# Optimization experiments

Measured on AMD Instinct MI355X. Metric: run time of the kernel, lower is better.

Reference implementation:

```python
import jax, jax.numpy as jnp
import numpy as np
from jax import lax

B, T, DE, DT = 64, 511, 400, 100
D = DE + DT              # encoder + tag embedding concat
S = T + 1                # head sentinel prepended
HG, HE, M = 384, 64, 32  # graph hidden, edge hidden, band width


def lstm_layer(x, h0, c0, Wih, Whh, bih, bhh):
    """x: [N, L, in] -> [N, L, H]; torch LSTM gate order (i, f, g, o)."""
    def step(carry, xt):
        h, c = carry
        gates = xt @ Wih.T + bih + h @ Whh.T + bhh
        i, f, g, o = jnp.split(gates, 4, axis=-1)
        c = jax.nn.sigmoid(f) * c + jax.nn.sigmoid(i) * jnp.tanh(g)
        h = jax.nn.sigmoid(o) * jnp.tanh(c)
        return (h, c), h
    _, ys = lax.scan(step, (h0, c0), jnp.swapaxes(x, 0, 1))
    return jnp.swapaxes(ys, 0, 1)


def setup_inputs() -> dict:
    key = jax.random.key(0)
    ks = jax.random.split(key, 32)
    def u(k, shape, h):
        s = 1.0 / np.sqrt(h)
        return jax.random.uniform(k, shape, jnp.float32, -s, s)
    return {
        "input": jax.random.normal(ks[0], (B, T, DE), jnp.float32),
        "tag_embeddings": jax.random.normal(ks[1], (B, T, DT), jnp.float32),
        "mask": jnp.ones((B, T), jnp.int32),
        "head_indices": jax.random.randint(ks[2], (B, T), 0, S),
        "head_sentinel": jax.random.normal(ks[3], (D,), jnp.float32),
        "bos_past": jnp.zeros((1,), jnp.float32),
        # graph LSTM (2 layers, dropout inactive at eval)
        "g_Wih0": u(ks[4], (4 * HG, D), HG),  "g_Whh0": u(ks[5], (4 * HG, HG), HG),
        "g_bih0": u(ks[6], (4 * HG,), HG),     "g_bhh0": u(ks[7], (4 * HG,), HG),
        "g_Wih1": u(ks[8], (4 * HG, HG), HG),  "g_Whh1": u(ks[9], (4 * HG, HG), HG),
        "g_bih1": u(ks[10], (4 * HG,), HG),    "g_bhh1": u(ks[11], (4 * HG,), HG),
        # edge LSTM past (2 layers, input size 1)
        "e_Wih0": u(ks[12], (4 * HE, 1), HE),  "e_Whh0": u(ks[13], (4 * HE, HE), HE),
        "e_bih0": u(ks[14], (4 * HE,), HE),    "e_bhh0": u(ks[15], (4 * HE,), HE),
        "e_Wih1": u(ks[16], (4 * HE, HE), HE), "e_Whh1": u(ks[17], (4 * HE, HE), HE),
        "e_bih1": u(ks[18], (4 * HE,), HE),    "e_bhh1": u(ks[19], (4 * HE,), HE),
        "g2e_W": u(ks[20], (HE, HG), HG),      "g2e_b": u(ks[21], (HE,), HG),
        "cls_W": u(ks[22], (1, HE), HE),       "cls_b": u(ks[23], (1,), HE),
        "ht_W": u(ks[24], (DT, HG), HG),       "ht_b": u(ks[25], (DT,), HG),
        "dt_W": u(ks[26], (DT, HG), HG),       "dt_b": u(ks[27], (DT,), HG),
    }


def reference(input, tag_embeddings, mask, head_indices, head_sentinel, bos_past,
              g_Wih0, g_Whh0, g_bih0, g_bhh0, g_Wih1, g_Whh1, g_bih1, g_bhh1,
              e_Wih0, e_Whh0, e_bih0, e_bhh0, e_Wih1, e_Whh1, e_bih1, e_bhh1,
              g2e_W, g2e_b, cls_W, cls_b, ht_W, ht_b, dt_W, dt_b):
    # --- sentinel prepend + adjust_for_sentinel ---
    x = jnp.concatenate([input, tag_embeddings], axis=-1)                      # [B,T,D]
    x = jnp.concatenate([jnp.broadcast_to(head_sentinel, (B, 1, D)), x], 1)    # [B,S,D]
    mask_s = jnp.concatenate([jnp.ones((B, 1), mask.dtype), mask], axis=1)
    heads = jnp.concatenate([jnp.zeros((B, 1), head_indices.dtype), head_indices], axis=1)
    # --- packed graph LSTM (2 layers, zero init); pad_packed zeros masked positions ---
    zg = jnp.zeros((B, HG), x.dtype)
    h = lstm_layer(x, zg, zg, g_Wih0, g_Whh0, g_bih0, g_bhh0)
    graph_state = lstm_layer(h, zg, zg, g_Wih1, g_Whh1, g_bih1, g_bhh1)        # [B,S,HG]
    graph_state = graph_state * mask_s[..., None].astype(graph_state.dtype)
    # --- edge_pass_train (split=False): teacher-forced banded edge LSTM ---
    proj = graph_state.reshape(B * S, HG) @ g2e_W.T + g2e_b                    # [B*S,HE]
    Lm = min(M, S)
    A_sq = jax.nn.one_hot(heads, S, dtype=jnp.float32)                         # adj_indices_to_adj_matrix
    A_in = A_sq[:, :, :Lm].reshape(B * S, Lm, 1)                               # make_adj_sequence band
    bos = jnp.broadcast_to(bos_past.reshape(1, 1, 1), (B * S, 1, 1))
    A_in = jnp.concatenate([bos, A_in], axis=1)                                # [B*S,Lm+1,1]
    ze = jnp.zeros((B * S, HE), proj.dtype)
    e = lstm_layer(A_in, proj, ze, e_Wih0, e_Whh0, e_bih0, e_bhh0)             # h0=proj per layer, c0=0
    e = lstm_layer(e, proj, ze, e_Wih1, e_Whh1, e_bih1, e_bhh1)
    edge_logits = e @ cls_W.T + cls_b                                          # [B*S,Lm+1,1]
    Ap = edge_logits[:, 1:, 0].reshape(B, S, Lm)                               # drop bos step
    # banded writeback: arc_logits[:, i, :min(S,M)] = Ap[:, i, :] for every i
    arc_logits = jnp.zeros((B, S, S), graph_state.dtype).at[:, :, :Lm].set(Ap)
    # --- tag feedforwards (dropout = identity at eval) ---
    head_tag = jax.nn.elu(graph_state @ ht_W.T + ht_b)
    dep_tag = jax.nn.elu(graph_state @ dt_W.T + dt_b)
    return arc_logits, head_tag, dep_tag
```

## Files before the change

kernel.cpp:

```cpp
#include <hip/hip_runtime.h>
#include <hip/hip_bf16.h>
#include <stdint.h>

#define BB   64
#define TT   511
#define SS   512
#define DD   500
#define KXP  512
#define HG   384
#define G4   1536
#define HE   64
#define E4   256
#define NSEQ (BB*SS)

typedef __hip_bfloat16 bf16;
typedef float  floatx4 __attribute__((ext_vector_type(4)));
typedef int    intx4   __attribute__((ext_vector_type(4)));
typedef __bf16 bfrag8  __attribute__((ext_vector_type(8)));

static __device__ __forceinline__ floatx4 MFMA16(bfrag8 a, bfrag8 b, floatx4 c){
  return __builtin_amdgcn_mfma_f32_16x16x32_bf16(a, b, c, 0, 0, 0);
}
static __device__ __forceinline__ float sigm_(float x){ return 1.f/(1.f + __expf(-x)); }
static __device__ __forceinline__ float tanh_(float x){
  x = fminf(fmaxf(x, -15.f), 15.f);
  float e = __expf(2.f*x);
  return (e - 1.f)/(e + 1.f);
}
static __device__ __forceinline__ float actv(float x, bool isg){
  float s = 1.f/(1.f + __expf(isg ? -2.f*x : -x));
  return isg ? (2.f*s - 1.f) : s;
}
static __device__ __forceinline__ float b2f(unsigned short u){
  union { unsigned int i; float f; } x; x.i = ((unsigned int)u)<<16; return x.f;
}
static __device__ __forceinline__ unsigned short f2bu(float f){
  bf16 b = __float2bfloat16(f);
  return *reinterpret_cast<unsigned short*>(&b);
}
static __device__ __forceinline__ bfrag8 asfrag(intx4 v){
  union { intx4 i; bfrag8 f; } u; u.i = v; return u.f;
}

static __device__ __forceinline__ bfrag8 ldfrag_coh(const bf16* p){
  unsigned long long u0 = __hip_atomic_load((const unsigned long long*)p,     __ATOMIC_RELAXED, __HIP_MEMORY_SCOPE_SYSTEM);
  unsigned long long u1 = __hip_atomic_load((const unsigned long long*)p + 1, __ATOMIC_RELAXED, __HIP_MEMORY_SCOPE_SYSTEM);
  union { unsigned long long u[2]; bfrag8 f; } x; x.u[0]=u0; x.u[1]=u1;
  return x.f;
}
static __device__ __forceinline__ void stpair_coh(bf16* p, float lo, float hi){
  unsigned int pk = (unsigned int)f2bu(lo) | ((unsigned int)f2bu(hi) << 16);
  __hip_atomic_store((unsigned int*)p, pk, __ATOMIC_RELAXED, __HIP_MEMORY_SCOPE_SYSTEM);
}

__global__ __launch_bounds__(256) void prep_x(const float* __restrict__ input,
    const float* __restrict__ tag, const float* __restrict__ sent,
    bf16* __restrict__ Xb)
{
  const size_t stp = (size_t)gridDim.x * blockDim.x;
  for (size_t i = (size_t)blockIdx.x*blockDim.x + threadIdx.x; i < (size_t)NSEQ*KXP; i += stp){
    int m = (int)(i >> 9), k = (int)(i & 511);
    int b = m >> 9, s = m & 511;
    float v;
    if (k >= DD)        v = 0.f;
    else if (s == 0)    v = sent[k];
    else if (k < 400)   v = input[(size_t)(b*TT + s-1)*400 + k];
    else                v = tag  [(size_t)(b*TT + s-1)*100 + (k-400)];
    Xb[i] = __float2bfloat16(v);
  }
}

__global__ __launch_bounds__(256) void prep_w(
  const float* __restrict__ gWih0, const float* __restrict__ gWhh0,
  const float* __restrict__ gbih0, const float* __restrict__ gbhh0,
  const float* __restrict__ gWih1, const float* __restrict__ gWhh1,
  const float* __restrict__ gbih1, const float* __restrict__ gbhh1,
  const float* __restrict__ eWih0, const float* __restrict__ eWhh0,
  const float* __restrict__ ebih0, const float* __restrict__ ebhh0,
  const float* __restrict__ eWih1, const float* __restrict__ eWhh1,
  const float* __restrict__ ebih1, const float* __restrict__ ebhh1,
  const float* __restrict__ g2eW, const float* __restrict__ htW, const float* __restrict__ dtW,
  bf16* __restrict__ W0i, bf16* __restrict__ W0r, bf16* __restrict__ W1c,
  float* __restrict__ gb0, float* __restrict__ gb1,
  bf16* __restrict__ eW0b, bf16* __restrict__ eW1ab, bf16* __restrict__ eW1bb,
  float* __restrict__ eb0, float* __restrict__ eb1, float* __restrict__ ew0cv,
  bf16* __restrict__ g2eWb, bf16* __restrict__ htWb, bf16* __restrict__ dtWb)
{
  const int st = blockIdx.x*blockDim.x + threadIdx.x;
  const int gs = gridDim.x*blockDim.x;
  for (int i=st; i<G4*KXP; i+=gs){ int n=i>>9, k=i&511; int j=n>>2, g=n&3;
      W0i[i] = __float2bfloat16(k<DD ? gWih0[(size_t)(g*HG+j)*DD+k] : 0.f); }
  for (int i=st; i<G4*HG; i+=gs){ int n=i/HG, k=i-n*HG; int j=n>>2, g=n&3;
      W0r[i] = __float2bfloat16(gWhh0[(size_t)(g*HG+j)*HG+k]); }
  for (int i=st; i<G4*768; i+=gs){ int n=i/768, k=i-n*768; int j=n>>2, g=n&3;
      W1c[i] = __float2bfloat16(k<HG ? gWih1[(size_t)(g*HG+j)*HG+k]
                                     : gWhh1[(size_t)(g*HG+j)*HG+(k-HG)]); }
  for (int i=st; i<G4; i+=gs){ int j=i>>2, g=i&3; int s=g*HG+j;
      gb0[i]=gbih0[s]+gbhh0[s]; gb1[i]=gbih1[s]+gbhh1[s]; }
  for (int i=st; i<E4*HE; i+=gs){ eW0b[i]=__float2bfloat16(eWhh0[i]);
      eW1ab[i]=__float2bfloat16(eWih1[i]); eW1bb[i]=__float2bfloat16(eWhh1[i]); }
  for (int i=st; i<E4; i+=gs){ eb0[i]=ebih0[i]+ebhh0[i]; eb1[i]=ebih1[i]+ebhh1[i];
      ew0cv[i]=eWih0[i]; }
  for (int i=st; i<HE*HG; i+=gs) g2eWb[i]=__float2bfloat16(g2eW[i]);
  for (int i=st; i<128*HG; i+=gs){
      htWb[i] = __float2bfloat16(i<100*HG ? htW[i] : 0.f);
      dtWb[i] = __float2bfloat16(i<100*HG ? dtW[i] : 0.f); }
}

template<int KTOT,int BN,int WAVES_M,int WAVES_N,int EPI>
__global__ __launch_bounds__(256) void gemm_mfma(
    const bf16* __restrict__ A, const bf16* __restrict__ Wt,
    const float* __restrict__ bias, const int* __restrict__ mask,
    void* __restrict__ outp, int Nreal)
{
  constexpr int WMT = 128/(WAVES_M*16);
  constexpr int WNT = BN /(WAVES_N*16);
  __shared__ alignas(16) bf16 As[128][32];
  __shared__ alignas(16) bf16 Bs[BN][32];
  const int tid = threadIdx.x;
  const int bm = blockIdx.x & 255, bn = blockIdx.x >> 8;
  const int m0 = bm*128, n0 = bn*BN;
  const int wid = tid>>6, l = tid&63, lj = l&15, lq = l>>4;
  const int wm = wid / WAVES_N, wn = wid % WAVES_N;
  floatx4 acc[WMT][WNT] = {};
  for (int k0 = 0; k0 < KTOT; k0 += 32){
    __syncthreads();
    for (int c = tid; c < 128*4; c += 256){
      int row = c>>2, ch = c&3;
      *(uint4*)&As[row][ch*8] = *(const uint4*)&A[(size_t)(m0+row)*KTOT + k0 + ch*8];
    }
    for (int c = tid; c < BN*4; c += 256){
      int row = c>>2, ch = c&3;
      *(uint4*)&Bs[row][ch*8] = *(const uint4*)&Wt[(size_t)(n0+row)*KTOT + k0 + ch*8];
    }
    __syncthreads();
    bfrag8 af[WMT]; bfrag8 bfr[WNT];
    #pragma unroll
    for (int mi=0;mi<WMT;++mi) af[mi]  = *(const bfrag8*)&As[wm*WMT*16 + mi*16 + lj][lq*8];
    #pragma unroll
    for (int ni=0;ni<WNT;++ni) bfr[ni] = *(const bfrag8*)&Bs[wn*WNT*16 + ni*16 + lj][lq*8];
    #pragma unroll
    for (int mi=0;mi<WMT;++mi)
      #pragma unroll
      for (int ni=0;ni<WNT;++ni)
        acc[mi][ni] = MFMA16(af[mi], bfr[ni], acc[mi][ni]);
  }
  #pragma unroll
  for (int mi=0;mi<WMT;++mi){
    #pragma unroll
    for (int ni=0;ni<WNT;++ni){
      #pragma unroll
      for (int r=0;r<4;++r){
        int grow = m0 + wm*WMT*16 + mi*16 + 4*lq + r;
        int gcol = n0 + wn*WNT*16 + ni*16 + lj;
        float v = acc[mi][ni][r];
        if (EPI == 0){
          v += bias[gcol];
          ((bf16*)outp)[(size_t)grow*Nreal + gcol] = __float2bfloat16(v);
        } else if (EPI == 3){
          v += bias[gcol];
          int s = grow & 511, b = grow >> 9;
          ((bf16*)outp)[((size_t)s*BB + b)*G4 + gcol] = __float2bfloat16(v);
        } else {
          int s = grow & 511, b = grow >> 9;
          float mk = (s==0) ? 1.f : (float)mask[b*TT + s - 1];
          v = v*mk + bias[gcol];
          if (EPI == 1){
            ((bf16*)outp)[(size_t)grow*Nreal + gcol] = __float2bfloat16(v);
          } else {
            v = v > 0.f ? v : expm1f(v);
            if (gcol < Nreal) ((float*)outp)[(size_t)grow*Nreal + gcol] = v;
          }
        }
      }
    }
  }
}

template<int IS1>
__device__ __forceinline__ void rnn_body(int bid, int tid,
    const bf16* __restrict__ G0t, const bf16* __restrict__ Wsrc,
    const float* __restrict__ gb1,
    bf16* __restrict__ h0seq, bf16* __restrict__ h1seq, unsigned int* __restrict__ flags)
{
  constexpr int KW = IS1 ? 768 : 384;
  constexpr int KF = IS1 ? 24 : 12;
  const int bl = IS1 ? bid-48 : bid;
  const int w = tid>>6, l = tid&63, lj = l&15, lq = l>>4;
  const int m0 = w*16;
  const int n0 = bl*32;
  const int a  = lj>>2;
  const int gl = l&3;
  const bool isg = (gl==2);

  intx4 Wr0[KF], Wr1[KF];
  #pragma unroll
  for (int kf=0; kf<KF; ++kf){
    Wr0[kf] = *(const intx4*)&Wsrc[(size_t)(n0 + lj)*KW      + kf*32 + lq*8];
    Wr1[kf] = *(const intx4*)&Wsrc[(size_t)(n0 + 16 + lj)*KW + kf*32 + lq*8];
  }
  #pragma unroll
  for (int kf=0; kf<KF; ++kf)
    asm volatile("" : "+v"(Wr0[kf]), "+v"(Wr1[kf]));

  float bi0 = 0.f, bi1 = 0.f;
  if (IS1){ bi0 = gb1[n0 + 4*a + gl]; bi1 = gb1[n0 + 16 + 4*a + gl]; }

  float c0s[4]={0,0,0,0}, c1s[4]={0,0,0,0};
  unsigned short g0pre[2][4];
  if (!IS1){
    #pragma unroll
    for (int nt=0;nt<2;++nt)
      #pragma unroll
      for (int r=0;r<4;++r)
        g0pre[nt][r] = *(const unsigned short*)&G0t[(size_t)(m0 + 4*lq + r)*G4 + n0 + nt*16 + 4*a + gl];
  }
  unsigned int* myflag = flags + (size_t)(((IS1?48:0) + bl)*4 + w)*16;
  unsigned int* f0p = flags + (size_t)((l)*4 + w)*16;
  unsigned int* f1p = flags + (size_t)((48 + l)*4 + w)*16;

  const int ITMAX = IS1 ? SS : (SS-1);
  for (int it=0; it<=ITMAX; ++it){
    if (it >= 1){
      const unsigned tgt = (unsigned)it;
      const bool need = (l < 48);
      while (true){
        bool ok = true;
        if (need){
          unsigned f0 = __hip_atomic_load(f0p, __ATOMIC_RELAXED, __HIP_MEMORY_SCOPE_AGENT);
          ok = (f0 >= tgt);
          if (IS1){
            unsigned f1 = __hip_atomic_load(f1p, __ATOMIC_RELAXED, __HIP_MEMORY_SCOPE_AGENT);
            ok = ok && (f1 >= tgt);
          }
        }
        if (__all(ok)) break;
        __builtin_amdgcn_s_sleep(1);
      }
      asm volatile("" ::: "memory");
    }
    if (!IS1 || it >= 1){
      const int t = IS1 ? it-1 : it;
      bfrag8 ha[KF];
      if (IS1){
        const bf16* hb0 = h0seq + ((size_t)t*BB + (m0+lj))*HG;
        #pragma unroll
        for (int kf=0;kf<12;++kf) ha[kf] = ldfrag_coh(hb0 + kf*32 + lq*8);
        if (t > 0){
          const bf16* hb1 = h1seq + ((size_t)(m0+lj)*SS + (t-1))*HG;
          #pragma unroll
          for (int kf=12;kf<24;++kf) ha[kf] = ldfrag_coh(hb1 + (kf-12)*32 + lq*8);
        }
      } else if (t > 0){
        const bf16* hb = h0seq + ((size_t)(t-1)*BB + (m0+lj))*HG;
        #pragma unroll
        for (int kf=0;kf<12;++kf) ha[kf] = ldfrag_coh(hb + kf*32 + lq*8);
      }
      floatx4 aA0={0,0,0,0}, aB0={0,0,0,0}, aA1={0,0,0,0}, aB1={0,0,0,0};
      if (IS1 || t > 0){
        #pragma unroll
        for (int kf=0;kf<12;++kf){
          if (kf&1){ aB0 = MFMA16(ha[kf], asfrag(Wr0[kf]), aB0); aB1 = MFMA16(ha[kf], asfrag(Wr1[kf]), aB1); }
          else     { aA0 = MFMA16(ha[kf], asfrag(Wr0[kf]), aA0); aA1 = MFMA16(ha[kf], asfrag(Wr1[kf]), aA1); }
        }
      }
      if (IS1 && t > 0){
        #pragma unroll
        for (int kf=12;kf<24;++kf){
          if (kf&1){ aB0 = MFMA16(ha[kf], asfrag(Wr0[kf]), aB0); aB1 = MFMA16(ha[kf], asfrag(Wr1[kf]), aB1); }
          else     { aA0 = MFMA16(ha[kf], asfrag(Wr0[kf]), aA0); aA1 = MFMA16(ha[kf], asfrag(Wr1[kf]), aA1); }
        }
      }
      const floatx4 s0 = aA0 + aB0, s1 = aA1 + aB1;
      #pragma unroll
      for (int nt=0; nt<2; ++nt){
        #pragma unroll
        for (int r=0; r<4; ++r){
          float x = nt ? s1[r] : s0[r];
          x += IS1 ? (nt ? bi1 : bi0) : b2f(g0pre[nt][r]);
          float av = actv(x, isg);
          float i_ = __shfl(av, (l&60)|0);
          float f_ = __shfl(av, (l&60)|1);
          float g_ = __shfl(av, (l&60)|2);
          float o_ = __shfl(av, (l&60)|3);
          float cp = nt ? c1s[r] : c0s[r];
          float c = f_*cp + i_*g_;
          if (nt) c1s[r] = c; else c0s[r] = c;
          float h = o_*tanh_(c);
          float hn = __shfl(h, l^4);
          if ((l&7) == 0){
            int bb = m0 + 4*lq + r;
            int jh = bl*8 + nt*4 + a;
            bf16* hp = IS1 ? (h1seq + ((size_t)bb*SS + t)*HG + jh)
                           : (h0seq + ((size_t)t*BB + bb)*HG + jh);
            stpair_coh(hp, h, hn);
          }
        }
      }
    }
    asm volatile("s_waitcnt vmcnt(0)" ::: "memory");
    if (l == 0)
      __hip_atomic_store(myflag, (unsigned)(it+1),
                         __ATOMIC_RELAXED, __HIP_MEMORY_SCOPE_AGENT);
    if (!IS1 && it+1 <= ITMAX){
      #pragma unroll
      for (int nt=0;nt<2;++nt)
        #pragma unroll
        for (int r=0;r<4;++r)
          g0pre[nt][r] = *(const unsigned short*)&G0t[((size_t)(it+1)*BB + m0 + 4*lq + r)*G4 + n0 + nt*16 + 4*a + gl];
    }
  }
}

__global__ __launch_bounds__(256,1) void graph_rnn(
    const bf16* __restrict__ G0t, const bf16* __restrict__ W0r, const bf16* __restrict__ W1c,
    const float* __restrict__ gb1, bf16* __restrict__ h0seq, bf16* __restrict__ h1seq,
    unsigned int* flags)
{
  if (blockIdx.x < 48) rnn_body<0>(blockIdx.x, threadIdx.x, G0t, W0r, gb1, h0seq, h1seq, flags);
  else                 rnn_body<1>(blockIdx.x, threadIdx.x, G0t, W1c, gb1, h0seq, h1seq, flags);
}

__global__ __launch_bounds__(256) void edge_lstm(
    const bf16* __restrict__ projb,
    const bf16* __restrict__ eW0b, const bf16* __restrict__ eW1ab, const bf16* __restrict__ eW1bb,
    const float* __restrict__ eb0, const float* __restrict__ eb1, const float* __restrict__ ew0c,
    const float* __restrict__ clsW, const float* __restrict__ clsb_p, const float* __restrict__ bos_p,
    const int* __restrict__ heads, float* __restrict__ arc)
{
  __shared__ alignas(16) bf16 hbuf0[16][72];
  __shared__ alignas(16) bf16 hbuf1[16][72];
  __shared__ float lbuf[4][16];
  const int tid = threadIdx.x, w = tid>>6, l = tid&63, lj = l&15, lq = l>>4;
  const int seq0 = blockIdx.x * 16;
  const int jglob = w*16 + lj;
  for (int i = tid; i < 16*64; i += 256){
    int sl = i >> 6, jj = i & 63;
    bf16 v = projb[(size_t)(seq0+sl)*HE + jj];
    hbuf0[sl][jj] = v; hbuf1[sl][jj] = v;
  }
  bfrag8 W0f[4][2], W1af[4][2], W1bf[4][2];
  #pragma unroll
  for (int g=0; g<4; ++g){
    #pragma unroll
    for (int kk=0; kk<2; ++kk){
      size_t offw = (size_t)(g*HE + jglob)*HE + kk*32 + lq*8;
      W0f [g][kk] = *(const bfrag8*)&eW0b [offw];
      W1af[g][kk] = *(const bfrag8*)&eW1ab[offw];
      W1bf[g][kk] = *(const bfrag8*)&eW1bb[offw];
    }
  }
  float ebr0[4], ebr1[4], ewr[4];
  #pragma unroll
  for (int g=0; g<4; ++g){ ebr0[g]=eb0[g*HE+jglob]; ebr1[g]=eb1[g*HE+jglob]; ewr[g]=ew0c[g*HE+jglob]; }
  const float clswj = clsW[jglob];
  const float bos = bos_p[0], clsb = clsb_p[0];
  int hd[4]; float c0r[4]={0,0,0,0}, c1r[4]={0,0,0,0};
  #pragma unroll
  for (int r=0;r<4;++r){
    int sq = seq0 + 4*lq + r;
    int b = sq >> 9, s = sq & 511;
    hd[r] = (s==0) ? 0 : heads[b*TT + s - 1];
  }
  __syncthreads();
  for (int j=0; j<33; ++j){
    floatx4 acc0[4] = {};
    bfrag8 a0[2];
    #pragma unroll
    for (int kk=0; kk<2; ++kk)
      a0[kk] = *(const bfrag8*)((const char*)&hbuf0[0][0] + lj*144 + kk*64 + lq*16);
    #pragma unroll
    for (int g=0; g<4; ++g)
      #pragma unroll
      for (int kk=0; kk<2; ++kk)
        acc0[g] = MFMA16(a0[kk], W0f[g][kk], acc0[g]);
    __syncthreads();
    float h0v[4];
    #pragma unroll
    for (int r=0;r<4;++r){
      float x = (j==0) ? bos : ((hd[r] == j-1) ? 1.f : 0.f);
      float pi = acc0[0][r] + ebr0[0] + x*ewr[0];
      float pf = acc0[1][r] + ebr0[1] + x*ewr[1];
      float pg = acc0[2][r] + ebr0[2] + x*ewr[2];
      float po = acc0[3][r] + ebr0[3] + x*ewr[3];
      float i_=sigm_(pi), f_=sigm_(pf), g_=tanh_(pg), o_=sigm_(po);
      c0r[r] = f_*c0r[r] + i_*g_;
      h0v[r] = o_*tanh_(c0r[r]);
    }
    #pragma unroll
    for (int r=0;r<4;++r) hbuf0[4*lq + r][jglob] = __float2bfloat16(h0v[r]);
    __syncthreads();
    floatx4 acc1[4] = {};
    bfrag8 a1[2], a2[2];
    #pragma unroll
    for (int kk=0;kk<2;++kk){
      a1[kk] = *(const bfrag8*)((const char*)&hbuf0[0][0] + lj*144 + kk*64 + lq*16);
      a2[kk] = *(const bfrag8*)((const char*)&hbuf1[0][0] + lj*144 + kk*64 + lq*16);
    }
    #pragma unroll
    for (int g=0; g<4; ++g){
      #pragma unroll
      for (int kk=0;kk<2;++kk){
        acc1[g] = MFMA16(a1[kk], W1af[g][kk], acc1[g]);
        acc1[g] = MFMA16(a2[kk], W1bf[g][kk], acc1[g]);
      }
    }
    __syncthreads();
    float p[4];
    #pragma unroll
    for (int r=0;r<4;++r){
      float pi = acc1[0][r] + ebr1[0];
      float pf = acc1[1][r] + ebr1[1];
      float pg = acc1[2][r] + ebr1[2];
      float po = acc1[3][r] + ebr1[3];
      float i_=sigm_(pi), f_=sigm_(pf), g_=tanh_(pg), o_=sigm_(po);
      c1r[r] = f_*c1r[r] + i_*g_;
      float h1 = o_*tanh_(c1r[r]);
      hbuf1[4*lq + r][jglob] = __float2bfloat16(h1);
      p[r] = h1 * clswj;
    }
    #pragma unroll
    for (int mk=1; mk<16; mk<<=1)
      #pragma unroll
      for (int r=0;r<4;++r) p[r] += __shfl_xor(p[r], mk, 64);
    if (lj == 0){
      #pragma unroll
      for (int r=0;r<4;++r) lbuf[w][4*lq + r] = p[r];
    }
    __syncthreads();
    if (tid < 16 && j >= 1){
      int sq = seq0 + tid;
      float v = lbuf[0][tid] + lbuf[1][tid] + lbuf[2][tid] + lbuf[3][tid] + clsb;
      arc[(size_t)sq*SS + (j-1)] = v;
    }
  }
}

extern "C" void kernel_launch(void* const* d_in, const int* in_sizes, int n_in,
                              void* d_out, int out_size, void* d_ws, size_t ws_size,
                              hipStream_t stream)
{
  const float* input = (const float*)d_in[0];
  const float* tag   = (const float*)d_in[1];
  const int*   mask  = (const int*)  d_in[2];
  const int*   heads = (const int*)  d_in[3];
  const float* sent  = (const float*)d_in[4];
  const float* bosp  = (const float*)d_in[5];
  const float* gWih0 = (const float*)d_in[6];
  const float* gWhh0 = (const float*)d_in[7];
  const float* gbih0 = (const float*)d_in[8];
  const float* gbhh0 = (const float*)d_in[9];
  const float* gWih1 = (const float*)d_in[10];
  const float* gWhh1 = (const float*)d_in[11];
  const float* gbih1 = (const float*)d_in[12];
  const float* gbhh1 = (const float*)d_in[13];
  const float* eWih0 = (const float*)d_in[14];
  const float* eWhh0 = (const float*)d_in[15];
  const float* ebih0 = (const float*)d_in[16];
  const float* ebhh0 = (const float*)d_in[17];
  const float* eWih1 = (const float*)d_in[18];
  const float* eWhh1 = (const float*)d_in[19];
  const float* ebih1 = (const float*)d_in[20];
  const float* ebhh1 = (const float*)d_in[21];
  const float* g2eW  = (const float*)d_in[22];
  const float* g2eb  = (const float*)d_in[23];
  const float* clsW  = (const float*)d_in[24];
  const float* clsb  = (const float*)d_in[25];
  const float* htW   = (const float*)d_in[26];
  const float* htb   = (const float*)d_in[27];
  const float* dtW   = (const float*)d_in[28];
  const float* dtb   = (const float*)d_in[29];

  char* wsb = (char*)d_ws;
  size_t off = 0;
  auto take = [&](size_t bytes)->char* {
    char* p = wsb + off;
    off = (off + bytes + 255) & ~(size_t)255;
    return p;
  };
  bf16*  Xb     = (bf16*) take((size_t)NSEQ*KXP*2);
  bf16*  W0i    = (bf16*) take((size_t)G4*KXP*2);
  bf16*  W0r    = (bf16*) take((size_t)G4*HG*2);
  bf16*  W1c    = (bf16*) take((size_t)G4*768*2);
  float* gb0i   = (float*)take(G4*4);
  float* gb1i   = (float*)take(G4*4);
  bf16*  G0t    = (bf16*) take((size_t)NSEQ*G4*2);
  bf16*  h0seq  = (bf16*) take((size_t)SS*BB*HG*2);
  bf16*  h1seq  = (bf16*) take((size_t)NSEQ*HG*2);
  unsigned int* flags = (unsigned int*)take(384*16*4);
  bf16*  projb  = (bf16*) take((size_t)NSEQ*HE*2);
  bf16*  eW0b   = (bf16*) take(E4*HE*2);
  bf16*  eW1ab  = (bf16*) take(E4*HE*2);
  bf16*  eW1bb  = (bf16*) take(E4*HE*2);
  float* eb0w   = (float*)take(E4*4);
  float* eb1w   = (float*)take(E4*4);
  float* ew0cw  = (float*)take(E4*4);
  bf16*  g2eWb  = (bf16*) take(HE*HG*2);
  bf16*  htWb   = (bf16*) take(128*HG*2);
  bf16*  dtWb   = (bf16*) take(128*HG*2);

  (void)hipMemsetAsync(d_out, 0, (size_t)16777216*4, stream);
  (void)hipMemsetAsync(flags, 0, 384*16*4, stream);

  prep_x<<<2048,256,0,stream>>>(input, tag, sent, Xb);
  prep_w<<<512,256,0,stream>>>(gWih0,gWhh0,gbih0,gbhh0,gWih1,gWhh1,gbih1,gbhh1,
                               eWih0,eWhh0,ebih0,ebhh0,eWih1,eWhh1,ebih1,ebhh1,
                               g2eW,htW,dtW,
                               W0i,W0r,W1c,gb0i,gb1i,eW0b,eW1ab,eW1bb,
                               eb0w,eb1w,ew0cw,g2eWb,htWb,dtWb);

  gemm_mfma<KXP,128,2,2,3><<<3072,256,0,stream>>>(Xb, W0i, gb0i, nullptr, (void*)G0t, G4);

  graph_rnn<<<96,256,0,stream>>>(G0t, W0r, W1c, gb1i, h0seq, h1seq, flags);

  gemm_mfma<HG,64,4,1,1><<<256,256,0,stream>>>(h1seq, g2eWb, g2eb, mask, (void*)projb, HE);

  edge_lstm<<<2048,256,0,stream>>>(projb, eW0b, eW1ab, eW1bb, eb0w, eb1w, ew0cw,
                                   clsW, clsb, bosp, heads, (float*)d_out);

  gemm_mfma<HG,128,2,2,2><<<256,256,0,stream>>>(h1seq, htWb, htb, mask,
      (void*)((float*)d_out + 16777216), 100);
  gemm_mfma<HG,128,2,2,2><<<256,256,0,stream>>>(h1seq, dtWb, dtb, mask,
      (void*)((float*)d_out + 16777216 + 3276800), 100);
}
```

Before: 4.936 ms.

## Overlap layer-0 input GEMM with recurrent LSTM via flags; fuse post GEMMs

Moves the layer-0 input-projection GEMM into the persistent graph_rnn launch as extra worker blocks that process timestep pairs in order. Each worker publishes a per-tile flag, and the recurrent blocks wait on those flags before reading G0t, so the projection overlaps the sequential recurrence instead of running before it. It also merges the three post-RNN GEMMs into a single launch and vectorises the prep_x and prep_w conversion loops. The risk is that correctness now depends on the RNN blocks being resident and progressing while they spin on flags, and there is extra flag polling and memory traffic from the system-scope stores.

After: 5.184 ms. 1.05x slower.

```diff
diff --git a/kernel.cpp b/kernel.cpp
--- a/kernel.cpp
+++ b/kernel.cpp
@@ -17,6 +17,7 @@
 typedef float  floatx4 __attribute__((ext_vector_type(4)));
 typedef int    intx4   __attribute__((ext_vector_type(4)));
 typedef __bf16 bfrag8  __attribute__((ext_vector_type(8)));
+typedef unsigned short ushort8 __attribute__((ext_vector_type(8)));
 
 static __device__ __forceinline__ floatx4 MFMA16(bfrag8 a, bfrag8 b, floatx4 c){
   return __builtin_amdgcn_mfma_f32_16x16x32_bf16(a, b, c, 0, 0, 0);
@@ -52,21 +53,49 @@
   unsigned int pk = (unsigned int)f2bu(lo) | ((unsigned int)f2bu(hi) << 16);
   __hip_atomic_store((unsigned int*)p, pk, __ATOMIC_RELAXED, __HIP_MEMORY_SCOPE_SYSTEM);
 }
+static __device__ __forceinline__ unsigned int ld32_sys(const bf16* p){
+  return __hip_atomic_load((const unsigned int*)p, __ATOMIC_RELAXED, __HIP_MEMORY_SCOPE_SYSTEM);
+}
+static __device__ __forceinline__ void st32_sys(bf16* p, unsigned int v){
+  __hip_atomic_store((unsigned int*)p, v, __ATOMIC_RELAXED, __HIP_MEMORY_SCOPE_SYSTEM);
+}
 
 __global__ __launch_bounds__(256) void prep_x(const float* __restrict__ input,
     const float* __restrict__ tag, const float* __restrict__ sent,
     bf16* __restrict__ Xb)
 {
+  const size_t N8 = (size_t)NSEQ*KXP/8;
   const size_t stp = (size_t)gridDim.x * blockDim.x;
-  for (size_t i = (size_t)blockIdx.x*blockDim.x + threadIdx.x; i < (size_t)NSEQ*KXP; i += stp){
-    int m = (int)(i >> 9), k = (int)(i & 511);
+  for (size_t i8 = (size_t)blockIdx.x*blockDim.x + threadIdx.x; i8 < N8; i8 += stp){
+    int m = (int)(i8 >> 6);
+    int k = ((int)i8 & 63) * 8;
     int b = m >> 9, s = m & 511;
-    float v;
-    if (k >= DD)        v = 0.f;
-    else if (s == 0)    v = sent[k];
-    else if (k < 400)   v = input[(size_t)(b*TT + s-1)*400 + k];
-    else                v = tag  [(size_t)(b*TT + s-1)*100 + (k-400)];
-    Xb[i] = __float2bfloat16(v);
+    float v[8];
+    if (s == 0){
+      #pragma unroll
+      for (int j=0;j<8;++j) v[j] = (k+j < DD) ? sent[k+j] : 0.f;
+    } else if (k < 400){
+      const float* src = input + (size_t)(b*TT + s-1)*400 + k;
+      float4 a = *(const float4*)src;
+      float4 c = *(const float4*)(src+4);
+      v[0]=a.x; v[1]=a.y; v[2]=a.z; v[3]=a.w; v[4]=c.x; v[5]=c.y; v[6]=c.z; v[7]=c.w;
+    } else if (k < 496){
+      const float* src = tag + (size_t)(b*TT + s-1)*100 + (k-400);
+      float4 a = *(const float4*)src;
+      float4 c = *(const float4*)(src+4);
+      v[0]=a.x; v[1]=a.y; v[2]=a.z; v[3]=a.w; v[4]=c.x; v[5]=c.y; v[6]=c.z; v[7]=c.w;
+    } else if (k == 496){
+      const float* src = tag + (size_t)(b*TT + s-1)*100 + 96;
+      float4 a = *(const float4*)src;
+      v[0]=a.x; v[1]=a.y; v[2]=a.z; v[3]=a.w; v[4]=0.f; v[5]=0.f; v[6]=0.f; v[7]=0.f;
+    } else {
+      #pragma unroll
+      for (int j=0;j<8;++j) v[j]=0.f;
+    }
+    ushort8 o;
+    #pragma unroll
+    for (int j=0;j<8;++j) o[j] = f2bu(v[j]);
+    *(ushort8*)&Xb[i8*8] = o;
   }
 }
 
@@ -88,27 +117,40 @@
 {
   const int st = blockIdx.x*blockDim.x + threadIdx.x;
   const int gs = gridDim.x*blockDim.x;
-  for (int i=st; i<G4*KXP; i+=gs){ int n=i>>9, k=i&511; int j=n>>2, g=n&3;
-      W0i[i] = __float2bfloat16(k<DD ? gWih0[(size_t)(g*HG+j)*DD+k] : 0.f); }
-  for (int i=st; i<G4*HG; i+=gs){ int n=i/HG, k=i-n*HG; int j=n>>2, g=n&3;
-      W0r[i] = __float2bfloat16(gWhh0[(size_t)(g*HG+j)*HG+k]); }
-  for (int i=st; i<G4*768; i+=gs){ int n=i/768, k=i-n*768; int j=n>>2, g=n&3;
-      W1c[i] = __float2bfloat16(k<HG ? gWih1[(size_t)(g*HG+j)*HG+k]
-                                     : gWhh1[(size_t)(g*HG+j)*HG+(k-HG)]); }
+  auto cvt4 = [](const float* s)->ushort4 {
+    float4 f = *(const float4*)s;
+    ushort4 u; u.x=f2bu(f.x); u.y=f2bu(f.y); u.z=f2bu(f.z); u.w=f2bu(f.w); return u;
+  };
+  for (int i4=st; i4<G4*KXP/4; i4+=gs){ int n=i4>>7, kk=(i4&127)*4; int j=n>>2, g=n&3;
+      ushort4 u;
+      if (kk < DD) u = cvt4(&gWih0[(size_t)(g*HG+j)*DD + kk]);
+      else { u.x=u.y=u.z=u.w=0; }
+      *(ushort4*)&W0i[(size_t)i4*4] = u; }
+  for (int i4=st; i4<G4*HG/4; i4+=gs){ int n=i4/96, kk=(i4%96)*4; int j=n>>2, g=n&3;
+      *(ushort4*)&W0r[(size_t)i4*4] = cvt4(&gWhh0[(size_t)(g*HG+j)*HG + kk]); }
+  for (int i4=st; i4<G4*768/4; i4+=gs){ int n=i4/192, kk=(i4%192)*4; int j=n>>2, g=n&3;
+      const float* s = (kk<HG) ? &gWih1[(size_t)(g*HG+j)*HG + kk]
+                               : &gWhh1[(size_t)(g*HG+j)*HG + (kk-HG)];
+      *(ushort4*)&W1c[(size_t)i4*4] = cvt4(s); }
   for (int i=st; i<G4; i+=gs){ int j=i>>2, g=i&3; int s=g*HG+j;
       gb0[i]=gbih0[s]+gbhh0[s]; gb1[i]=gbih1[s]+gbhh1[s]; }
-  for (int i=st; i<E4*HE; i+=gs){ eW0b[i]=__float2bfloat16(eWhh0[i]);
-      eW1ab[i]=__float2bfloat16(eWih1[i]); eW1bb[i]=__float2bfloat16(eWhh1[i]); }
+  for (int i4=st; i4<E4*HE/4; i4+=gs){
+      *(ushort4*)&eW0b [(size_t)i4*4] = cvt4(&eWhh0[(size_t)i4*4]);
+      *(ushort4*)&eW1ab[(size_t)i4*4] = cvt4(&eWih1[(size_t)i4*4]);
+      *(ushort4*)&eW1bb[(size_t)i4*4] = cvt4(&eWhh1[(size_t)i4*4]); }
   for (int i=st; i<E4; i+=gs){ eb0[i]=ebih0[i]+ebhh0[i]; eb1[i]=ebih1[i]+ebhh1[i];
       ew0cv[i]=eWih0[i]; }
-  for (int i=st; i<HE*HG; i+=gs) g2eWb[i]=__float2bfloat16(g2eW[i]);
-  for (int i=st; i<128*HG; i+=gs){
-      htWb[i] = __float2bfloat16(i<100*HG ? htW[i] : 0.f);
-      dtWb[i] = __float2bfloat16(i<100*HG ? dtW[i] : 0.f); }
+  for (int i4=st; i4<HE*HG/4; i4+=gs)
+      *(ushort4*)&g2eWb[(size_t)i4*4] = cvt4(&g2eW[(size_t)i4*4]);
+  for (int i4=st; i4<128*HG/4; i4+=gs){ int i=i4*4;
+      ushort4 uh, ud;
+      if (i < 100*HG){ uh = cvt4(&htW[i]); ud = cvt4(&dtW[i]); }
+      else { uh.x=uh.y=uh.z=uh.w=0; ud=uh; }
+      *(ushort4*)&htWb[i] = uh; *(ushort4*)&dtWb[i] = ud; }
 }
 
 template<int KTOT,int BN,int WAVES_M,int WAVES_N,int EPI>
-__global__ __launch_bounds__(256) void gemm_mfma(
+__device__ __forceinline__ void gemm_body(int bid,
     const bf16* __restrict__ A, const bf16* __restrict__ Wt,
     const float* __restrict__ bias, const int* __restrict__ mask,
     void* __restrict__ outp, int Nreal)
@@ -118,7 +160,7 @@
   __shared__ alignas(16) bf16 As[128][32];
   __shared__ alignas(16) bf16 Bs[BN][32];
   const int tid = threadIdx.x;
-  const int bm = blockIdx.x & 255, bn = blockIdx.x >> 8;
+  const int bm = bid & 255, bn = bid >> 8;
   const int m0 = bm*128, n0 = bn*BN;
   const int wid = tid>>6, l = tid&63, lj = l&15, lq = l>>4;
   const int wm = wid / WAVES_N, wn = wid % WAVES_N;
@@ -154,34 +196,99 @@
         int grow = m0 + wm*WMT*16 + mi*16 + 4*lq + r;
         int gcol = n0 + wn*WNT*16 + ni*16 + lj;
         float v = acc[mi][ni][r];
-        if (EPI == 0){
-          v += bias[gcol];
+        int s = grow & 511, b = grow >> 9;
+        float mk = (s==0) ? 1.f : (float)mask[b*TT + s - 1];
+        v = v*mk + bias[gcol];
+        if (EPI == 1){
           ((bf16*)outp)[(size_t)grow*Nreal + gcol] = __float2bfloat16(v);
-        } else if (EPI == 3){
-          v += bias[gcol];
-          int s = grow & 511, b = grow >> 9;
-          ((bf16*)outp)[((size_t)s*BB + b)*G4 + gcol] = __float2bfloat16(v);
         } else {
-          int s = grow & 511, b = grow >> 9;
-          float mk = (s==0) ? 1.f : (float)mask[b*TT + s - 1];
-          v = v*mk + bias[gcol];
-          if (EPI == 1){
-            ((bf16*)outp)[(size_t)grow*Nreal + gcol] = __float2bfloat16(v);
-          } else {
-            v = v > 0.f ? v : expm1f(v);
-            if (gcol < Nreal) ((float*)outp)[(size_t)grow*Nreal + gcol] = v;
-          }
+          v = v > 0.f ? v : expm1f(v);
+          if (gcol < Nreal) ((float*)outp)[(size_t)grow*Nreal + gcol] = v;
         }
       }
     }
   }
+}
+
+__global__ __launch_bounds__(256) void post_fused(
+    const bf16* __restrict__ h1seq,
+    const bf16* __restrict__ g2eWb, const float* __restrict__ g2eb,
+    const bf16* __restrict__ htWb, const float* __restrict__ htb,
+    const bf16* __restrict__ dtWb, const float* __restrict__ dtb,
+    const int* __restrict__ mask,
+    bf16* __restrict__ projb, float* __restrict__ out_ht, float* __restrict__ out_dt)
+{
+  const int b = blockIdx.x;
+  if (b < 256)      gemm_body<HG,64,4,1,1>(b,     h1seq, g2eWb, g2eb, mask, (void*)projb, HE);
+  else if (b < 512) gemm_body<HG,128,2,2,2>(b-256, h1seq, htWb,  htb,  mask, (void*)out_ht, 100);
+  else              gemm_body<HG,128,2,2,2>(b-512, h1seq, dtWb,  dtb,  mask, (void*)out_dt, 100);
+}
+
+__device__ void g0_worker(int gbid,
+    const bf16* __restrict__ Xb, const bf16* __restrict__ W0i,
+    const float* __restrict__ gb0, bf16* __restrict__ G0t,
+    unsigned int* __restrict__ g0flags)
+{
+  __shared__ alignas(16) bf16 As[128][32];
+  __shared__ alignas(16) bf16 Bs[128][32];
+  const int tid = threadIdx.x;
+  const int bm = gbid & 255, bn = gbid >> 8;
+  const int s0 = bm*2, n0 = bn*128;
+  const int wid = tid>>6, l = tid&63, lj = l&15, lq = l>>4;
+  const int wm = wid >> 1, wn = wid & 1;
+  floatx4 acc[4][4] = {};
+  for (int k0 = 0; k0 < KXP; k0 += 32){
+    __syncthreads();
+    for (int c = tid; c < 128*4; c += 256){
+      int row = c>>2, ch = c&3;
+      int grow = ((row>>1)<<9) + s0 + (row&1);
+      *(uint4*)&As[row][ch*8] = *(const uint4*)&Xb[(size_t)grow*KXP + k0 + ch*8];
+      *(uint4*)&Bs[row][ch*8] = *(const uint4*)&W0i[(size_t)(n0+row)*KXP + k0 + ch*8];
+    }
+    __syncthreads();
+    bfrag8 af[4], bfr[4];
+    #pragma unroll
+    for (int mi=0;mi<4;++mi) af[mi]  = *(const bfrag8*)&As[wm*64 + mi*16 + lj][lq*8];
+    #pragma unroll
+    for (int ni=0;ni<4;++ni) bfr[ni] = *(const bfrag8*)&Bs[wn*64 + ni*16 + lj][lq*8];
+    #pragma unroll
+    for (int mi=0;mi<4;++mi)
+      #pragma unroll
+      for (int ni=0;ni<4;++ni)
+        acc[mi][ni] = MFMA16(af[mi], bfr[ni], acc[mi][ni]);
+  }
+  #pragma unroll
+  for (int mi=0;mi<4;++mi){
+    #pragma unroll
+    for (int ni=0;ni<4;++ni){
+      #pragma unroll
+      for (int r=0;r<4;++r){
+        int trow = wm*64 + mi*16 + 4*lq + r;
+        int gcol = n0 + wn*64 + ni*16 + lj;
+        float v = acc[mi][ni][r] + gb0[gcol];
+        float vhi = __shfl_xor(v, 1);
+        if ((lj & 1) == 0){
+          int s = s0 + (trow & 1), b = trow >> 1;
+          bf16* p = G0t + ((size_t)s*BB + b)*G4 + gcol;
+          unsigned int pk = (unsigned)f2bu(v) | ((unsigned)f2bu(vhi) << 16);
+          st32_sys(p, pk);
+        }
+      }
+    }
+  }
+  asm volatile("s_waitcnt vmcnt(0)" ::: "memory");
+  __syncthreads();
+  if (tid == 0)
+    __hip_atomic_store(&g0flags[(size_t)(bm*12 + bn)*16], 1u,
+                       __ATOMIC_RELAXED, __HIP_MEMORY_SCOPE_AGENT);
 }
 
 template<int IS1>
 __device__ __forceinline__ void rnn_body(int bid, int tid,
     const bf16* __restrict__ G0t, const bf16* __restrict__ Wsrc,
     const float* __restrict__ gb1,
-    bf16* __restrict__ h0seq, bf16* __restrict__ h1seq, unsigned int* __restrict__ flags)
+    bf16* __restrict__ h0seq, bf16* __restrict__ h1seq,
+    unsigned int* __restrict__ flags, unsigned int* __restrict__ g0flags)
 {
   constexpr int KW = IS1 ? 768 : 384;
   constexpr int KF = IS1 ? 24 : 12;
@@ -207,13 +314,17 @@
   if (IS1){ bi0 = gb1[n0 + 4*a + gl]; bi1 = gb1[n0 + 16 + 4*a + gl]; }
 
   float c0s[4]={0,0,0,0}, c1s[4]={0,0,0,0};
-  unsigned short g0pre[2][4];
+  unsigned int g0pre[2][4];
   if (!IS1){
+    unsigned int* gfl = g0flags + (size_t)(0*12 + (bl>>2))*16;
+    while (__hip_atomic_load(gfl, __ATOMIC_RELAXED, __HIP_MEMORY_SCOPE_AGENT) < 1u)
+      __builtin_amdgcn_s_sleep(2);
+    asm volatile("" ::: "memory");
     #pragma unroll
     for (int nt=0;nt<2;++nt)
       #pragma unroll
       for (int r=0;r<4;++r)
-        g0pre[nt][r] = *(const unsigned short*)&G0t[(size_t)(m0 + 4*lq + r)*G4 + n0 + nt*16 + 4*a + gl];
+        g0pre[nt][r] = ld32_sys(&G0t[(size_t)(m0 + 4*lq + r)*G4 + n0 + nt*16 + 4*a + (gl&2)]);
   }
   unsigned int* myflag = flags + (size_t)(((IS1?48:0) + bl)*4 + w)*16;
   unsigned int* f0p = flags + (size_t)((l)*4 + w)*16;
@@ -223,16 +334,20 @@
   for (int it=0; it<=ITMAX; ++it){
     if (it >= 1){
       const unsigned tgt = (unsigned)it;
-      const bool need = (l < 48);
+      unsigned int* gp = nullptr;
+      if (!IS1){ int bm = (it+1)>>1; if (bm>255) bm=255;
+                 gp = g0flags + (size_t)(bm*12 + (bl>>2))*16; }
       while (true){
         bool ok = true;
-        if (need){
+        if (l < 48){
           unsigned f0 = __hip_atomic_load(f0p, __ATOMIC_RELAXED, __HIP_MEMORY_SCOPE_AGENT);
           ok = (f0 >= tgt);
           if (IS1){
             unsigned f1 = __hip_atomic_load(f1p, __ATOMIC_RELAXED, __HIP_MEMORY_SCOPE_AGENT);
             ok = ok && (f1 >= tgt);
           }
+        } else if (!IS1 && l == 48){
+          ok = (__hip_atomic_load(gp, __ATOMIC_RELAXED, __HIP_MEMORY_SCOPE_AGENT) >= 1u);
         }
         if (__all(ok)) break;
         __builtin_amdgcn_s_sleep(1);
@@ -277,7 +392,11 @@
         #pragma unroll
         for (int r=0; r<4; ++r){
           float x = nt ? s1[r] : s0[r];
-          x += IS1 ? (nt ? bi1 : bi0) : b2f(g0pre[nt][r]);
+          if (IS1) x += (nt ? bi1 : bi0);
+          else {
+            unsigned u = g0pre[nt][r];
+            x += b2f((gl&1) ? (unsigned short)(u>>16) : (unsigned short)(u&0xffff));
+          }
           float av = actv(x, isg);
           float i_ = __shfl(av, (l&60)|0);
           float f_ = __shfl(av, (l&60)|1);
@@ -307,7 +426,7 @@
       for (int nt=0;nt<2;++nt)
         #pragma unroll
         for (int r=0;r<4;++r)
-          g0pre[nt][r] = *(const unsigned short*)&G0t[((size_t)(it+1)*BB + m0 + 4*lq + r)*G4 + n0 + nt*16 + 4*a + gl];
+          g0pre[nt][r] = ld32_sys(&G0t[((size_t)(it+1)*BB + m0 + 4*lq + r)*G4 + n0 + nt*16 + 4*a + (gl&2)]);
     }
   }
 }
@@ -315,10 +434,13 @@
 __global__ __launch_bounds__(256,1) void graph_rnn(
     const bf16* __restrict__ G0t, const bf16* __restrict__ W0r, const bf16* __restrict__ W1c,
     const float* __restrict__ gb1, bf16* __restrict__ h0seq, bf16* __restrict__ h1seq,
-    unsigned int* flags)
-{
-  if (blockIdx.x < 48) rnn_body<0>(blockIdx.x, threadIdx.x, G0t, W0r, gb1, h0seq, h1seq, flags);
-  else                 rnn_body<1>(blockIdx.x, threadIdx.x, G0t, W1c, gb1, h0seq, h1seq, flags);
+    unsigned int* flags, unsigned int* g0flags,
+    const bf16* __restrict__ Xb, const bf16* __restrict__ W0i, const float* __restrict__ gb0)
+{
+  const int bid = blockIdx.x;
+  if (bid < 48)      rnn_body<0>(bid, threadIdx.x, G0t, W0r, gb1, h0seq, h1seq, flags, g0flags);
+  else if (bid < 96) rnn_body<1>(bid, threadIdx.x, G0t, W1c, gb1, h0seq, h1seq, flags, g0flags);
+  else               g0_worker(bid-96, Xb, W0i, gb0, (bf16*)G0t, g0flags);
 }
 
 __global__ __launch_bounds__(256) void edge_lstm(
@@ -487,7 +609,8 @@
   bf16*  G0t    = (bf16*) take((size_t)NSEQ*G4*2);
   bf16*  h0seq  = (bf16*) take((size_t)SS*BB*HG*2);
   bf16*  h1seq  = (bf16*) take((size_t)NSEQ*HG*2);
-  unsigned int* flags = (unsigned int*)take(384*16*4);
+  unsigned int* flags   = (unsigned int*)take(384*16*4);
+  unsigned int* g0flags = (unsigned int*)take(3072*16*4);
   bf16*  projb  = (bf16*) take((size_t)NSEQ*HE*2);
   bf16*  eW0b   = (bf16*) take(E4*HE*2);
   bf16*  eW1ab  = (bf16*) take(E4*HE*2);
@@ -501,6 +624,7 @@
 
   (void)hipMemsetAsync(d_out, 0, (size_t)16777216*4, stream);
   (void)hipMemsetAsync(flags, 0, 384*16*4, stream);
+  (void)hipMemsetAsync(g0flags, 0, 3072*16*4, stream);
 
   prep_x<<<2048,256,0,stream>>>(input, tag, sent, Xb);
   prep_w<<<512,256,0,stream>>>(gWih0,gWhh0,gbih0,gbhh0,gWih1,gWhh1,gbih1,gbhh1,
@@ -509,17 +633,13 @@
                                W0i,W0r,W1c,gb0i,gb1i,eW0b,eW1ab,eW1bb,
                                eb0w,eb1w,ew0cw,g2eWb,htWb,dtWb);
 
-  gemm_mfma<KXP,128,2,2,3><<<3072,256,0,stream>>>(Xb, W0i, gb0i, nullptr, (void*)G0t, G4);
-
-  graph_rnn<<<96,256,0,stream>>>(G0t, W0r, W1c, gb1i, h0seq, h1seq, flags);
-
-  gemm_mfma<HG,64,4,1,1><<<256,256,0,stream>>>(h1seq, g2eWb, g2eb, mask, (void*)projb, HE);
+  graph_rnn<<<96+3072,256,0,stream>>>(G0t, W0r, W1c, gb1i, h0seq, h1seq,
+                                      flags, g0flags, Xb, W0i, gb0i);
+
+  post_fused<<<768,256,0,stream>>>(h1seq, g2eWb, g2eb, htWb, htb, dtWb, dtb, mask,
+                                   projb, (float*)d_out + 16777216,
+                                   (float*)d_out + 16777216 + 3276800);
 
   edge_lstm<<<2048,256,0,stream>>>(projb, eW0b, eW1ab, eW1bb, eb0w, eb1w, ew0cw,
                                    clsW, clsb, bosp, heads, (float*)d_out);
-
-  gemm_mfma<HG,128,2,2,2><<<256,256,0,stream>>>(h1seq, htWb, htb, mask,
-      (void*)((float*)d_out + 16777216), 100);
-  gemm_mfma<HG,128,2,2,2><<<256,256,0,stream>>>(h1seq, dtWb, dtb, mask,
-      (void*)((float*)d_out + 16777216 + 3276800), 100);
-}
+}
```
